# Kernel optimization log

Measured on AMD Instinct MI355X. Metric: run time of the kernel, lower is better.

## Reference

```python
import jax, jax.numpy as jnp
import numpy as np

N, DIM, HID, NCLS, E = 100000, 256, 16, 64, 3200000
NEG_SLOPE = 0.2


def setup_inputs() -> dict:
    key = jax.random.key(0)
    ks = jax.random.split(key, 10)
    x = jax.random.normal(ks[0], (N, DIM), dtype=jnp.float32)
    edge_index = jax.random.randint(ks[1], (2, E), 0, N, dtype=jnp.int64)
    # GATConv params (heads=1): glorot-ish scaled normals
    W1 = jax.random.normal(ks[2], (DIM, HID), dtype=jnp.float32) / np.sqrt(DIM)
    a_src1 = jax.random.normal(ks[3], (HID,), dtype=jnp.float32) / np.sqrt(HID)
    a_dst1 = jax.random.normal(ks[4], (HID,), dtype=jnp.float32) / np.sqrt(HID)
    b1 = jnp.zeros((HID,), dtype=jnp.float32)
    W2 = jax.random.normal(ks[5], (HID, NCLS), dtype=jnp.float32) / np.sqrt(HID)
    a_src2 = jax.random.normal(ks[6], (NCLS,), dtype=jnp.float32) / np.sqrt(NCLS)
    a_dst2 = jax.random.normal(ks[7], (NCLS,), dtype=jnp.float32) / np.sqrt(NCLS)
    b2 = jnp.zeros((NCLS,), dtype=jnp.float32)
    return {"x": x, "edge_index": edge_index, "W1": W1, "a_src1": a_src1,
            "a_dst1": a_dst1, "b1": b1, "W2": W2, "a_src2": a_src2,
            "a_dst2": a_dst2, "b2": b2}


def gat_conv(x, src, dst, W, a_s, a_d, b, n):
    # PyG GATConv, heads=1: h = x W; e_ij = LeakyReLU(a_s.h_j + a_d.h_i)
    h = x @ W                                   # [N, out]
    alpha_s = h @ a_s                           # [N]
    alpha_d = h @ a_d                           # [N]
    e = jax.nn.leaky_relu(alpha_s[src] + alpha_d[dst], NEG_SLOPE)  # [E]
    # softmax over edges grouped by destination node
    m = jax.ops.segment_max(e, dst, num_segments=n)
    m = jnp.where(jnp.isfinite(m), m, 0.0)
    ee = jnp.exp(e - m[dst])
    denom = jax.ops.segment_sum(ee, dst, num_segments=n)
    alpha = ee / denom[dst]                     # self-loops guarantee denom > 0
    out = jax.ops.segment_sum(h[src] * alpha[:, None], dst, num_segments=n)
    return out + b


def reference(x, edge_index, W1, a_src1, a_dst1, b1, W2, a_src2, a_dst2, b2):
    n = x.shape[0]
    loop = jnp.arange(n, dtype=edge_index.dtype)
    src = jnp.concatenate([edge_index[0], loop])  # add self-loops (PyG default)
    dst = jnp.concatenate([edge_index[1], loop])
    h = jax.nn.relu(gat_conv(x, src, dst, W1, a_src1, a_dst1, b1, n))
    # F.dropout treated as identity (inference / deterministic reference)
    out = gat_conv(h, src, dst, W2, a_src2, a_dst2, b2, n)
    return jax.nn.log_softmax(out, axis=1)
```

## Files before the change

kernel.cpp:

```cpp
#include <hip/hip_runtime.h>
#include <hip/hip_fp16.h>


#define DIM 256
#define HID 16
#define NCLS 64
#define NEG 0.2f
#define P1_CHUNK 4096
#define KITER 16
#define CAP 8704

typedef _Float16 f16x8 __attribute__((ext_vector_type(8)));
typedef float f32x4 __attribute__((ext_vector_type(4)));

__device__ __forceinline__ float lrelu(float v) { return v >= 0.f ? v : NEG * v; }

__device__ __forceinline__ uint4 pack_half8(const float* v) {
    __half2 p0 = __floats2half2_rn(v[0], v[1]);
    __half2 p1 = __floats2half2_rn(v[2], v[3]);
    __half2 p2 = __floats2half2_rn(v[4], v[5]);
    __half2 p3 = __floats2half2_rn(v[6], v[7]);
    return make_uint4(*(unsigned*)&p0, *(unsigned*)&p1, *(unsigned*)&p2, *(unsigned*)&p3);
}

__device__ __forceinline__ void unpack_half8(uint4 u, float* f) {
    float2 f0 = __half22float2(*(__half2*)&u.x);
    float2 f1 = __half22float2(*(__half2*)&u.y);
    float2 f2 = __half22float2(*(__half2*)&u.z);
    float2 f3 = __half22float2(*(__half2*)&u.w);
    f[0] = f0.x; f[1] = f0.y; f[2] = f1.x; f[3] = f1.y;
    f[4] = f2.x; f[5] = f2.y; f[6] = f3.x; f[7] = f3.y;
}

__global__ void vsd_kernel(const float* __restrict__ W2, const float* __restrict__ as2,
                           const float* __restrict__ ad2, float* __restrict__ vsd,
                           int* __restrict__ bkt_cnt, int* __restrict__ bkt_cur, int capb) {
    int t = threadIdx.x;
    bkt_cnt[t] = 0;
    bkt_cur[t] = capb ? t * capb : 0;
    if (t < 32) {
        int j = t & 15;
        const float* a = (t < 16) ? as2 : ad2;
        float s = 0.f;
        for (int c = 0; c < NCLS; ++c) s += W2[j * NCLS + c] * a[c];
        vsd[t] = s;
    }
}


__global__ __launch_bounds__(256) void p0_hist(const int* __restrict__ dst, int E,
                                               int* __restrict__ bkt_cnt) {
    __shared__ int hist[512];
    int t = threadIdx.x;
    for (int i = t; i < 512; i += 256) hist[i] = 0;
    __syncthreads();
    int base = blockIdx.x * P1_CHUNK;
#pragma unroll
    for (int k = 0; k < KITER; ++k) {
        int idx = base + k * 256 + t;
        if (idx < E) atomicAdd(&hist[dst[idx] >> 8], 1);
    }
    __syncthreads();
    for (int i = t; i < 512; i += 256)
        if (hist[i]) atomicAdd(&bkt_cnt[i], hist[i]);
}

__global__ void scanb(int* __restrict__ bkt_cnt, int* __restrict__ bkt_cur,
                      int* __restrict__ bkt_base, int nb) {
    __shared__ int lds[512];
    int t = threadIdx.x;
    int v = (t < nb) ? bkt_cnt[t] : 0;
    lds[t] = v;
    __syncthreads();
    for (int o = 1; o < 512; o <<= 1) {
        int x = (t >= o) ? lds[t - o] : 0;
        __syncthreads();
        lds[t] += x;
        __syncthreads();
    }
    if (t < nb) {
        int e = lds[t] - v;
        bkt_base[t] = e;
        bkt_cur[t] = e;
    }
}

struct H1S {
    _Float16 w1t[16][264];
    _Float16 hst[4][16][16];
};

__global__ __launch_bounds__(256) void p1h1_kernel(
    const int* __restrict__ ei, int E, int* __restrict__ bkt_cur,
    int* __restrict__ coarse, int nS, int h1blk, int capb,
    const float* __restrict__ x, const float* __restrict__ W1,
    uint4* __restrict__ h1h, int n) {
    __shared__ union __align__(16) { int hist[512]; H1S h1; } sm;
    int t = threadIdx.x;
    int bid = blockIdx.x;
    int total = nS + h1blk;
    int f0 = (int)(((long long)bid * h1blk) / total);
    int f1 = (int)(((long long)(bid + 1) * h1blk) / total);
    if (f1 == f0) {
        int sb = bid - f0;
        int base = sb * P1_CHUNK;
        int sarr[KITER], darr[KITER];
        for (int i = t; i < 512; i += 256) sm.hist[i] = 0;
        bool e4 = ((E & 3) == 0);
#pragma unroll
        for (int k = 0; k < KITER / 4; ++k) {
            int idx = base + (k * 256 + t) * 4;
            if (e4 && idx + 3 < E) {
                int4 s4 = *(const int4*)&ei[idx];
                int4 d4 = *(const int4*)&ei[E + idx];
                sarr[4 * k] = s4.x; sarr[4 * k + 1] = s4.y;
                sarr[4 * k + 2] = s4.z; sarr[4 * k + 3] = s4.w;
                darr[4 * k] = d4.x; darr[4 * k + 1] = d4.y;
                darr[4 * k + 2] = d4.z; darr[4 * k + 3] = d4.w;
            } else {
#pragma unroll
                for (int j = 0; j < 4; ++j) {
                    int id2 = idx + j;
                    if (id2 < E) { sarr[4 * k + j] = ei[id2]; darr[4 * k + j] = ei[E + id2]; }
                    else darr[4 * k + j] = -1;
                }
            }
        }
        __syncthreads();
#pragma unroll
        for (int k = 0; k < KITER; ++k)
            if (darr[k] >= 0) atomicAdd(&sm.hist[darr[k] >> 8], 1);
        __syncthreads();
        for (int b = t; b < 512; b += 256) {
            int c = sm.hist[b];
            sm.hist[b] = c ? atomicAdd(&bkt_cur[b], c) : 0;
        }
        __syncthreads();
#pragma unroll
        for (int k = 0; k < KITER; ++k) {
            int d = darr[k];
            if (d >= 0) {
                int bk = d >> 8;
                int pos = atomicAdd(&sm.hist[bk], 1);
                if (capb) pos = min(pos, (bk + 1) * capb - 1);
                coarse[pos] = (sarr[k] << 8) | (d & 255);
            }
        }
    } else {
        int hb = f0;
        {
            const float* row = W1 + t * HID;
#pragma unroll
            for (int nn2 = 0; nn2 < 16; ++nn2)
                sm.h1.w1t[nn2][t] = (_Float16)row[nn2];
        }
        __syncthreads();
        int lane = t & 63, wave = t >> 6;
        int q = lane >> 4, nn = lane & 15;
#pragma unroll 1
        for (int it = 0; it < 4; ++it) {
            int nb = hb * 256 + wave * 64 + it * 16;
            int node = nb + nn;
            const float* xr = x + (size_t)min(node, n - 1) * DIM;
            float4 st[16];
#pragma unroll
            for (int s = 0; s < 8; ++s) {
                int kb = s * 32 + q * 8;
                st[2 * s]     = *(const float4*)(xr + kb);
                st[2 * s + 1] = *(const float4*)(xr + kb + 4);
            }
            f32x4 acc = {0.f, 0.f, 0.f, 0.f};
#pragma unroll
            for (int s = 0; s < 8; ++s) {
                int kb = s * 32 + q * 8;
                f16x8 bf = *(const f16x8*)&sm.h1.w1t[nn][kb];
                float4 a0 = st[2 * s], a1 = st[2 * s + 1];
                f16x8 af;
                af[0] = (_Float16)a0.x; af[1] = (_Float16)a0.y;
                af[2] = (_Float16)a0.z; af[3] = (_Float16)a0.w;
                af[4] = (_Float16)a1.x; af[5] = (_Float16)a1.y;
                af[6] = (_Float16)a1.z; af[7] = (_Float16)a1.w;
                acc = __builtin_amdgcn_mfma_f32_16x16x32_f16(af, bf, acc, 0, 0, 0);
            }
            if (nb < n) {
#pragma unroll
                for (int r = 0; r < 4; ++r)
                    sm.h1.hst[wave][q * 4 + r][nn] = (_Float16)acc[r];
                __builtin_amdgcn_s_waitcnt(0);
                if (lane < 32) {
                    int nl = lane >> 1, jq = lane & 1;
                    int nd = nb + nl;
                    if (nd < n)
                        h1h[(size_t)nd * 2 + jq] = *(const uint4*)&sm.h1.hst[wave][nl][jq * 8];
                }
            }
        }
    }
}

__global__ __launch_bounds__(1024) void p2_fine(const int* __restrict__ coarse,
                                                const int* __restrict__ bkt_base,
                                                const int* __restrict__ bkt_cnt,
                                                const int* __restrict__ bkt_cur,
                                                int* __restrict__ csr, int* __restrict__ row_ptr,
                                                int* __restrict__ deg, int n, int capb) {
    __shared__ int cnt[256];
    __shared__ int off[256];
    __shared__ int csr_loc[CAP];
    int b = blockIdx.x;
    int t = threadIdx.x;
    int m, wbase;
    if (capb) {
        int* sc = csr_loc;
        if (t < 512) sc[t] = bkt_cur[t] - t * capb;
        __syncthreads();
        for (int o = 1; o < 512; o <<= 1) {
            int xg = (t >= o && t < 512) ? sc[t - o] : 0;
            __syncthreads();
            if (t < 512) sc[t] += xg;
            __syncthreads();
        }
        m = bkt_cur[b] - b * capb;
        wbase = sc[b] - m;
        __syncthreads();
    } else {
        m = bkt_cnt[b];
        wbase = bkt_base[b];
    }
    int rbase = capb ? b * capb : wbase;
    if (t < 256) cnt[t] = 0;
    __syncthreads();
    for (int i = t; i < m; i += 1024) atomicAdd(&cnt[coarse[rbase + i] & 255], 1);
    __syncthreads();
    int v = 0;
    if (t < 256) { v = cnt[t]; off[t] = v; }
    __syncthreads();
    for (int o = 1; o < 256; o <<= 1) {
        int xg = (t >= o && t < 256) ? off[t - o] : 0;
        __syncthreads();
        if (t < 256) off[t] += xg;
        __syncthreads();
    }
    if (t < 256) {
        int excl = off[t] - v;
        int node = b * 256 + t;
        if (node < n) {
            row_ptr[node] = wbase + excl;
            deg[node] = v;
        }
        cnt[t] = excl;
    }
    __syncthreads();
    if (m <= CAP) {
        for (int i = t; i < m; i += 1024) {
            int rec = coarse[rbase + i];
            int pos = atomicAdd(&cnt[rec & 255], 1);
            csr_loc[pos] = rec >> 8;
        }
        __syncthreads();
        for (int i = t; i < m; i += 1024) csr[wbase + i] = csr_loc[i];
    } else {
        for (int i = t; i < m; i += 1024) {
            int rec = coarse[rbase + i];
            int pos = atomicAdd(&cnt[rec & 255], 1);
            csr[wbase + pos] = rec >> 8;
        }
    }
}


__device__ __forceinline__ void agg_core(
    const uint4* __restrict__ hh, const float* aw, const float* dw,
    int node, int start, int cnt, const int* __restrict__ csr,
    int eq, int jq, float* acc, float* hs, float& denomv) {
    unpack_half8(hh[(size_t)node * 2 + jq], hs);
    float asn = 0.f, adn = 0.f;
#pragma unroll
    for (int i = 0; i < 8; ++i) { asn += hs[i] * aw[i]; adn += hs[i] * dw[i]; }
    asn += __shfl_xor(asn, 1, 64);
    adn += __shfl_xor(adn, 1, 64);
    float adi = adn;
    float w0 = __expf(lrelu(asn + adi));
    float w0s = (eq == 0) ? w0 : 0.f;
#pragma unroll
    for (int i = 0; i < 8; ++i) acc[i] = w0s * hs[i];
    float denom = w0s;
    int s0 = (eq < cnt)      ? csr[start + eq]      : node;
    int s1 = (8 + eq < cnt)  ? csr[start + 8 + eq]  : node;
    int s2 = (16 + eq < cnt) ? csr[start + 16 + eq] : node;
    int s3 = (24 + eq < cnt) ? csr[start + 24 + eq] : node;
    uint4 u0 = hh[(size_t)s0 * 2 + jq];
    uint4 u1 = hh[(size_t)s1 * 2 + jq];
    uint4 u2 = hh[(size_t)s2 * 2 + jq];
    uint4 u3 = hh[(size_t)s3 * 2 + jq];
#pragma unroll 1
    for (int q0 = 0; q0 < cnt; q0 += 32) {
        int nq = q0 + 32;
        int t0 = (nq + eq < cnt)      ? csr[start + nq + eq]      : node;
        int t1 = (nq + 8 + eq < cnt)  ? csr[start + nq + 8 + eq]  : node;
        int t2 = (nq + 16 + eq < cnt) ? csr[start + nq + 16 + eq] : node;
        int t3 = (nq + 24 + eq < cnt) ? csr[start + nq + 24 + eq] : node;
        uint4 v0 = hh[(size_t)t0 * 2 + jq];
        uint4 v1 = hh[(size_t)t1 * 2 + jq];
        uint4 v2 = hh[(size_t)t2 * 2 + jq];
        uint4 v3 = hh[(size_t)t3 * 2 + jq];
        float h[8], p, wv;
        unpack_half8(u0, h);
        p = 0.f;
#pragma unroll
        for (int i = 0; i < 8; ++i) p += h[i] * aw[i];
        p += __shfl_xor(p, 1, 64);
        wv = (q0 + eq < cnt) ? __expf(lrelu(p + adi)) : 0.f;
        denom += wv;
#pragma unroll
        for (int i = 0; i < 8; ++i) acc[i] += wv * h[i];
        unpack_half8(u1, h);
        p = 0.f;
#pragma unroll
        for (int i = 0; i < 8; ++i) p += h[i] * aw[i];
        p += __shfl_xor(p, 1, 64);
        wv = (q0 + 8 + eq < cnt) ? __expf(lrelu(p + adi)) : 0.f;
        denom += wv;
#pragma unroll
        for (int i = 0; i < 8; ++i) acc[i] += wv * h[i];
        unpack_half8(u2, h);
        p = 0.f;
#pragma unroll
        for (int i = 0; i < 8; ++i) p += h[i] * aw[i];
        p += __shfl_xor(p, 1, 64);
        wv = (q0 + 16 + eq < cnt) ? __expf(lrelu(p + adi)) : 0.f;
        denom += wv;
#pragma unroll
        for (int i = 0; i < 8; ++i) acc[i] += wv * h[i];
        unpack_half8(u3, h);
        p = 0.f;
#pragma unroll
        for (int i = 0; i < 8; ++i) p += h[i] * aw[i];
        p += __shfl_xor(p, 1, 64);
        wv = (q0 + 24 + eq < cnt) ? __expf(lrelu(p + adi)) : 0.f;
        denom += wv;
#pragma unroll
        for (int i = 0; i < 8; ++i) acc[i] += wv * h[i];
        u0 = v0; u1 = v1; u2 = v2; u3 = v3;
    }
#pragma unroll
    for (int m = 2; m <= 8; m <<= 1) {
#pragma unroll
        for (int i = 0; i < 8; ++i) acc[i] += __shfl_xor(acc[i], m, 64);
        denom += __shfl_xor(denom, m, 64);
    }
    denomv = denom;
}

__global__ __launch_bounds__(256) void agg1_kernel(
    const uint4* __restrict__ hh,
    const int* __restrict__ row_ptr, const int* __restrict__ deg, const int* __restrict__ csr,
    const float* __restrict__ as1, const float* __restrict__ ad1,
    const float* __restrict__ bias, uint4* __restrict__ outh, int n) {
    int t = threadIdx.x;
    int node = blockIdx.x * 16 + (t >> 4);
    if (node >= n) return;
    int lg = t & 15, jq = lg & 1, eq = lg >> 1;
    float aw[8], dw[8];
#pragma unroll
    for (int i = 0; i < 8; ++i) { aw[i] = as1[jq * 8 + i]; dw[i] = ad1[jq * 8 + i]; }
    float acc[8], hs[8];
    float denom;
    agg_core(hh, aw, dw, node, row_ptr[node], deg[node], csr, eq, jq, acc, hs, denom);
    float inv = 1.f / denom;
    float val[8];
#pragma unroll
    for (int i = 0; i < 8; ++i) val[i] = fmaxf(acc[i] * inv + bias[jq * 8 + i], 0.f);
    if (eq == 0) outh[(size_t)node * 2 + jq] = pack_half8(val);
}

__global__ __launch_bounds__(256) void agg2_final_kernel(
    const uint4* __restrict__ hh,
    const int* __restrict__ row_ptr, const int* __restrict__ deg, const int* __restrict__ csr,
    const float* __restrict__ vsd,
    const float* __restrict__ W2, const float* __restrict__ b2,
    float* __restrict__ out, int n) {
    __shared__ float a2s[16 * HID];
    __shared__ float w2s[HID * NCLS];
    __shared__ float b2s[NCLS];
    int t = threadIdx.x;
    for (int i = t; i < HID * NCLS; i += 256) w2s[i] = W2[i];
    if (t < NCLS) b2s[t] = b2[t];
    int g = t >> 4;
    int node = blockIdx.x * 16 + g;
    int lg = t & 15, jq = lg & 1, eq = lg >> 1;
    if (node < n) {
        float aw[8], dw[8];
#pragma unroll
        for (int i = 0; i < 8; ++i) { aw[i] = vsd[jq * 8 + i]; dw[i] = vsd[16 + jq * 8 + i]; }
        float acc[8], hs[8];
        float denom;
        agg_core(hh, aw, dw, node, row_ptr[node], deg[node], csr, eq, jq, acc, hs, denom);
        float inv = 1.f / denom;
        if (eq == 0) {
            float* dst = &a2s[g * HID + jq * 8];
            *(float4*)dst = make_float4(acc[0] * inv, acc[1] * inv, acc[2] * inv, acc[3] * inv);
            *(float4*)(dst + 4) = make_float4(acc[4] * inv, acc[5] * inv, acc[6] * inv, acc[7] * inv);
        }
    }
    __syncthreads();
    int wv = t >> 6;
    int c = t & 63;
#pragma unroll
    for (int i = 0; i < 4; ++i) {
        int nl = i * 4 + wv;
        int gn = blockIdx.x * 16 + nl;
        if (gn >= n) continue;
        const float* ar = &a2s[nl * HID];
        float v = b2s[c];
#pragma unroll
        for (int j = 0; j < HID; ++j) v += ar[j] * w2s[j * NCLS + c];
        float mx = v;
#pragma unroll
        for (int off = 1; off < 64; off <<= 1) mx = fmaxf(mx, __shfl_xor(mx, off, 64));
        float ex = __expf(v - mx);
        float s = ex;
#pragma unroll
        for (int off = 1; off < 64; off <<= 1) s += __shfl_xor(s, off, 64);
        out[(size_t)gn * NCLS + c] = (v - mx) - __logf(s);
    }
}

extern "C" void kernel_launch(void* const* d_in, const int* in_sizes, int n_in,
                              void* d_out, int out_size, void* d_ws, size_t ws_size,
                              hipStream_t stream) {
    const float* x    = (const float*)d_in[0];
    const int*   ei   = (const int*)d_in[1];
    const float* W1   = (const float*)d_in[2];
    const float* a_s1 = (const float*)d_in[3];
    const float* a_d1 = (const float*)d_in[4];
    const float* b1   = (const float*)d_in[5];
    const float* W2   = (const float*)d_in[6];
    const float* a_s2 = (const float*)d_in[7];
    const float* a_d2 = (const float*)d_in[8];
    const float* b2   = (const float*)d_in[9];
    float* out = (float*)d_out;

    const int N = in_sizes[0] / DIM;
    const int E = in_sizes[1] / 2;
    const int NB = (N + 255) >> 8;
    const int nS = (E + P1_CHUNK - 1) / P1_CHUNK;
    const int h1blk = (N + 255) / 256;

    char* p = (char*)d_ws;
    auto alloc = [&](size_t bytes) {
        char* r = p;
        p += (bytes + 255) & ~(size_t)255;
        return r;
    };
    int*   bkt_cnt  = (int*)alloc(512 * 4);
    int*   bkt_base = (int*)alloc(512 * 4);
    int*   bkt_cur  = (int*)alloc(512 * 4);
    int*   csr      = (int*)alloc((size_t)E * 4);
    int*   row_ptr  = (int*)alloc((size_t)N * 4);
    int*   deg      = (int*)alloc((size_t)N * 4);
    float* vsd      = (float*)alloc(32 * 4);
    uint4* h1h      = (uint4*)alloc((size_t)N * 32);
    uint4* hreluh   = (uint4*)alloc((size_t)N * 32);

    int capb = 10240;
    size_t used = (size_t)(p - (char*)d_ws);
    size_t pad_bytes = (size_t)512 * capb * 4;
    int* coarse;
    if (ws_size - used >= pad_bytes) {
        coarse = (int*)alloc(pad_bytes);
    } else {
        capb = 0;
        coarse = (int*)alloc((size_t)E * 4);
    }

    vsd_kernel<<<1, 512, 0, stream>>>(W2, a_s2, a_d2, vsd, bkt_cnt, bkt_cur, capb);
    if (!capb) {
        p0_hist<<<nS, 256, 0, stream>>>(ei + E, E, bkt_cnt);
        scanb<<<1, 512, 0, stream>>>(bkt_cnt, bkt_cur, bkt_base, NB);
    }
    p1h1_kernel<<<nS + h1blk, 256, 0, stream>>>(ei, E, bkt_cur, coarse, nS, h1blk, capb,
                                                x, W1, h1h, N);
    p2_fine<<<NB, 1024, 0, stream>>>(coarse, bkt_base, bkt_cnt, bkt_cur,
                                     csr, row_ptr, deg, N, capb);
    agg1_kernel<<<(N + 15) / 16, 256, 0, stream>>>(h1h, row_ptr, deg, csr,
                                                   a_s1, a_d1, b1, hreluh, N);
    agg2_final_kernel<<<(N + 15) / 16, 256, 0, stream>>>(hreluh, row_ptr, deg, csr,
                                                         vsd, W2, b2, out, N);
}
```

Before: 289.2 us.

## Fuse fine CSR bucketing with layer-1 aggregation reading neighbor lists from LDS

```diff
diff --git a/kernel.cpp b/kernel.cpp
--- a/kernel.cpp
+++ b/kernel.cpp
@@ -198,80 +198,10 @@
     }
 }
 
-__global__ __launch_bounds__(1024) void p2_fine(const int* __restrict__ coarse,
-                                                const int* __restrict__ bkt_base,
-                                                const int* __restrict__ bkt_cnt,
-                                                const int* __restrict__ bkt_cur,
-                                                int* __restrict__ csr, int* __restrict__ row_ptr,
-                                                int* __restrict__ deg, int n, int capb) {
-    __shared__ int cnt[256];
-    __shared__ int off[256];
-    __shared__ int csr_loc[CAP];
-    int b = blockIdx.x;
-    int t = threadIdx.x;
-    int m, wbase;
-    if (capb) {
-        int* sc = csr_loc;
-        if (t < 512) sc[t] = bkt_cur[t] - t * capb;
-        __syncthreads();
-        for (int o = 1; o < 512; o <<= 1) {
-            int xg = (t >= o && t < 512) ? sc[t - o] : 0;
-            __syncthreads();
-            if (t < 512) sc[t] += xg;
-            __syncthreads();
-        }
-        m = bkt_cur[b] - b * capb;
-        wbase = sc[b] - m;
-        __syncthreads();
-    } else {
-        m = bkt_cnt[b];
-        wbase = bkt_base[b];
-    }
-    int rbase = capb ? b * capb : wbase;
-    if (t < 256) cnt[t] = 0;
-    __syncthreads();
-    for (int i = t; i < m; i += 1024) atomicAdd(&cnt[coarse[rbase + i] & 255], 1);
-    __syncthreads();
-    int v = 0;
-    if (t < 256) { v = cnt[t]; off[t] = v; }
-    __syncthreads();
-    for (int o = 1; o < 256; o <<= 1) {
-        int xg = (t >= o && t < 256) ? off[t - o] : 0;
-        __syncthreads();
-        if (t < 256) off[t] += xg;
-        __syncthreads();
-    }
-    if (t < 256) {
-        int excl = off[t] - v;
-        int node = b * 256 + t;
-        if (node < n) {
-            row_ptr[node] = wbase + excl;
-            deg[node] = v;
-        }
-        cnt[t] = excl;
-    }
-    __syncthreads();
-    if (m <= CAP) {
-        for (int i = t; i < m; i += 1024) {
-            int rec = coarse[rbase + i];
-            int pos = atomicAdd(&cnt[rec & 255], 1);
-            csr_loc[pos] = rec >> 8;
-        }
-        __syncthreads();
-        for (int i = t; i < m; i += 1024) csr[wbase + i] = csr_loc[i];
-    } else {
-        for (int i = t; i < m; i += 1024) {
-            int rec = coarse[rbase + i];
-            int pos = atomicAdd(&cnt[rec & 255], 1);
-            csr[wbase + pos] = rec >> 8;
-        }
-    }
-}
-
 
 __device__ __forceinline__ void agg_core(
     const uint4* __restrict__ hh, const float* aw, const float* dw,
-    int node, int start, int cnt, const int* __restrict__ csr,
+    int node, int start, int cnt, const int* csr,
     int eq, int jq, float* acc, float* hs, float& denomv) {
     unpack_half8(hh[(size_t)node * 2 + jq], hs);
     float asn = 0.f, adn = 0.f;
@@ -352,26 +282,101 @@
     denomv = denom;
 }
 
-__global__ __launch_bounds__(256) void agg1_kernel(
-    const uint4* __restrict__ hh,
-    const int* __restrict__ row_ptr, const int* __restrict__ deg, const int* __restrict__ csr,
-    const float* __restrict__ as1, const float* __restrict__ ad1,
-    const float* __restrict__ bias, uint4* __restrict__ outh, int n) {
-    int t = threadIdx.x;
-    int node = blockIdx.x * 16 + (t >> 4);
-    if (node >= n) return;
+__global__ __launch_bounds__(1024) void p2agg1_kernel(
+    const int* __restrict__ coarse, const int* __restrict__ bkt_base,
+    const int* __restrict__ bkt_cnt, const int* __restrict__ bkt_cur,
+    int* __restrict__ csr, int* __restrict__ row_ptr, int* __restrict__ deg,
+    int n, int capb,
+    const uint4* __restrict__ hh, const float* __restrict__ as1,
+    const float* __restrict__ ad1, const float* __restrict__ bias,
+    uint4* __restrict__ outh) {
+    __shared__ int cnt[256];
+    __shared__ int off[256];
+    __shared__ int lstart[256];
+    __shared__ int ldeg[256];
+    __shared__ int csr_loc[CAP];
+    int b = blockIdx.x;
+    int t = threadIdx.x;
+    int m, wbase;
+    if (capb) {
+        int* sc = csr_loc;
+        if (t < 512) sc[t] = bkt_cur[t] - t * capb;
+        __syncthreads();
+        for (int o = 1; o < 512; o <<= 1) {
+            int xg = (t >= o && t < 512) ? sc[t - o] : 0;
+            __syncthreads();
+            if (t < 512) sc[t] += xg;
+            __syncthreads();
+        }
+        m = bkt_cur[b] - b * capb;
+        wbase = sc[b] - m;
+        __syncthreads();
+    } else {
+        m = bkt_cnt[b];
+        wbase = bkt_base[b];
+    }
+    int rbase = capb ? b * capb : wbase;
+    if (t < 256) cnt[t] = 0;
+    __syncthreads();
+    for (int i = t; i < m; i += 1024) atomicAdd(&cnt[coarse[rbase + i] & 255], 1);
+    __syncthreads();
+    int v = 0;
+    if (t < 256) { v = cnt[t]; off[t] = v; }
+    __syncthreads();
+    for (int o = 1; o < 256; o <<= 1) {
+        int xg = (t >= o && t < 256) ? off[t - o] : 0;
+        __syncthreads();
+        if (t < 256) off[t] += xg;
+        __syncthreads();
+    }
+    bool inlds = (m <= CAP);
+    if (t < 256) {
+        int excl = off[t] - v;
+        int node = b * 256 + t;
+        if (node < n) {
+            row_ptr[node] = wbase + excl;
+            deg[node] = v;
+        }
+        lstart[t] = excl;
+        ldeg[t] = v;
+        cnt[t] = excl;
+    }
+    __syncthreads();
+    if (inlds) {
+        for (int i = t; i < m; i += 1024) {
+            int rec = coarse[rbase + i];
+            int pos = atomicAdd(&cnt[rec & 255], 1);
+            csr_loc[pos] = rec >> 8;
+        }
+        __syncthreads();
+        for (int i = t; i < m; i += 1024) csr[wbase + i] = csr_loc[i];
+    } else {
+        for (int i = t; i < m; i += 1024) {
+            int rec = coarse[rbase + i];
+            int pos = atomicAdd(&cnt[rec & 255], 1);
+            csr[wbase + pos] = rec >> 8;
+        }
+        __syncthreads();
+    }
     int lg = t & 15, jq = lg & 1, eq = lg >> 1;
+    const int* csrp = inlds ? (const int*)csr_loc : (const int*)(csr + wbase);
     float aw[8], dw[8];
 #pragma unroll
     for (int i = 0; i < 8; ++i) { aw[i] = as1[jq * 8 + i]; dw[i] = ad1[jq * 8 + i]; }
-    float acc[8], hs[8];
-    float denom;
-    agg_core(hh, aw, dw, node, row_ptr[node], deg[node], csr, eq, jq, acc, hs, denom);
-    float inv = 1.f / denom;
-    float val[8];
-#pragma unroll
-    for (int i = 0; i < 8; ++i) val[i] = fmaxf(acc[i] * inv + bias[jq * 8 + i], 0.f);
-    if (eq == 0) outh[(size_t)node * 2 + jq] = pack_half8(val);
+#pragma unroll 1
+    for (int pass = 0; pass < 4; ++pass) {
+        int nl = pass * 64 + (t >> 4);
+        int node = b * 256 + nl;
+        if (node >= n) continue;
+        float acc[8], hs[8];
+        float denom;
+        agg_core(hh, aw, dw, node, lstart[nl], ldeg[nl], csrp, eq, jq, acc, hs, denom);
+        float inv = 1.f / denom;
+        float val[8];
+#pragma unroll
+        for (int i = 0; i < 8; ++i) val[i] = fmaxf(acc[i] * inv + bias[jq * 8 + i], 0.f);
+        if (eq == 0) outh[(size_t)node * 2 + jq] = pack_half8(val);
+    }
 }
 
 __global__ __launch_bounds__(256) void agg2_final_kernel(
@@ -481,10 +486,9 @@
     }
     p1h1_kernel<<<nS + h1blk, 256, 0, stream>>>(ei, E, bkt_cur, coarse, nS, h1blk, capb,
                                                 x, W1, h1h, N);
-    p2_fine<<<NB, 1024, 0, stream>>>(coarse, bkt_base, bkt_cnt, bkt_cur,
-                                     csr, row_ptr, deg, N, capb);
-    agg1_kernel<<<(N + 15) / 16, 256, 0, stream>>>(h1h, row_ptr, deg, csr,
-                                                   a_s1, a_d1, b1, hreluh, N);
+    p2agg1_kernel<<<NB, 1024, 0, stream>>>(coarse, bkt_base, bkt_cnt, bkt_cur,
+                                           csr, row_ptr, deg, N, capb,
+                                           h1h, a_s1, a_d1, b1, hreluh);
     agg2_final_kernel<<<(N + 15) / 16, 256, 0, stream>>>(hreluh, row_ptr, deg, csr,
                                                          vsd, W2, b2, out, N);
 }
```

Measured after the change: 300.2 us. +3.8%, slower.

## Replace two-level bucket sort CSR build with per-node atomic histogram and scatter

Applied to the files above, without the earlier changes.

```diff
diff --git a/kernel.cpp b/kernel.cpp
--- a/kernel.cpp
+++ b/kernel.cpp
@@ -6,9 +6,8 @@
 #define HID 16
 #define NCLS 64
 #define NEG 0.2f
-#define P1_CHUNK 4096
-#define KITER 16
-#define CAP 8704
+#define P1_CHUNK 2048
+#define KITER 8
 
 typedef _Float16 f16x8 __attribute__((ext_vector_type(8)));
 typedef float f32x4 __attribute__((ext_vector_type(4)));
@@ -32,13 +31,14 @@
     f[4] = f2.x; f[5] = f2.y; f[6] = f3.x; f[7] = f3.y;
 }
 
-__global__ void vsd_kernel(const float* __restrict__ W2, const float* __restrict__ as2,
-                           const float* __restrict__ ad2, float* __restrict__ vsd,
-                           int* __restrict__ bkt_cnt, int* __restrict__ bkt_cur, int capb) {
-    int t = threadIdx.x;
-    bkt_cnt[t] = 0;
-    bkt_cur[t] = capb ? t * capb : 0;
-    if (t < 32) {
+__global__ __launch_bounds__(1024) void vsd_zero_kernel(
+    const float* __restrict__ W2, const float* __restrict__ as2,
+    const float* __restrict__ ad2, float* __restrict__ vsd,
+    int* __restrict__ deg, int n) {
+    int i = blockIdx.x * 1024 + threadIdx.x;
+    if (i < n) deg[i] = 0;
+    if (blockIdx.x == 0 && threadIdx.x < 32) {
+        int t = threadIdx.x;
         int j = t & 15;
         const float* a = (t < 16) ? as2 : ad2;
         float s = 0.f;
@@ -47,41 +47,60 @@
     }
 }
 
-
-__global__ __launch_bounds__(256) void p0_hist(const int* __restrict__ dst, int E,
-                                               int* __restrict__ bkt_cnt) {
-    __shared__ int hist[512];
+__global__ __launch_bounds__(1024) void hist_kernel(const int* __restrict__ dst, int E,
+                                                    int* __restrict__ deg) {
+    int i4 = (blockIdx.x * 1024 + threadIdx.x) * 4;
+    if (i4 + 3 < E) {
+        int4 d4 = *(const int4*)&dst[i4];
+        atomicAdd(&deg[d4.x], 1);
+        atomicAdd(&deg[d4.y], 1);
+        atomicAdd(&deg[d4.z], 1);
+        atomicAdd(&deg[d4.w], 1);
+    } else {
+        for (int j = 0; j < 4; ++j)
+            if (i4 + j < E) atomicAdd(&deg[dst[i4 + j]], 1);
+    }
+}
+
+__global__ __launch_bounds__(1024) void scan1_kernel(const int* __restrict__ deg,
+                                                     int* __restrict__ row_ptr,
+                                                     int* __restrict__ btot, int n) {
+    __shared__ int arr[1024];
     int t = threadIdx.x;
-    for (int i = t; i < 512; i += 256) hist[i] = 0;
+    int i = blockIdx.x * 1024 + t;
+    int v = (i < n) ? deg[i] : 0;
+    arr[t] = v;
     __syncthreads();
-    int base = blockIdx.x * P1_CHUNK;
-#pragma unroll
-    for (int k = 0; k < KITER; ++k) {
-        int idx = base + k * 256 + t;
-        if (idx < E) atomicAdd(&hist[dst[idx] >> 8], 1);
-    }
+    for (int o = 1; o < 1024; o <<= 1) {
+        int x = (t >= o) ? arr[t - o] : 0;
+        __syncthreads();
+        arr[t] += x;
+        __syncthreads();
+    }
+    if (i < n) row_ptr[i] = arr[t] - v;
+    if (t == 1023) btot[blockIdx.x] = arr[1023];
+}
+
+__global__ __launch_bounds__(1024) void finalize_kernel(const int* __restrict__ btot,
+                                                        int* __restrict__ row_ptr,
+                                                        int* __restrict__ cursor,
+                                                        int n, int nblk) {
+    __shared__ int bs[128];
+    int t = threadIdx.x;
+    if (t < 128) bs[t] = (t < nblk) ? btot[t] : 0;
     __syncthreads();
-    for (int i = t; i < 512; i += 256)
-        if (hist[i]) atomicAdd(&bkt_cnt[i], hist[i]);
-}
-
-__global__ void scanb(int* __restrict__ bkt_cnt, int* __restrict__ bkt_cur,
-                      int* __restrict__ bkt_base, int nb) {
-    __shared__ int lds[512];
-    int t = threadIdx.x;
-    int v = (t < nb) ? bkt_cnt[t] : 0;
-    lds[t] = v;
-    __syncthreads();
-    for (int o = 1; o < 512; o <<= 1) {
-        int x = (t >= o) ? lds[t - o] : 0;
+    for (int o = 1; o < 128; o <<= 1) {
+        int x = (t >= o && t < 128) ? bs[t - o] : 0;
         __syncthreads();
-        lds[t] += x;
+        if (t < 128) bs[t] += x;
         __syncthreads();
     }
-    if (t < nb) {
-        int e = lds[t] - v;
-        bkt_base[t] = e;
-        bkt_cur[t] = e;
+    int base = (blockIdx.x == 0) ? 0 : bs[blockIdx.x - 1];
+    int i = blockIdx.x * 1024 + t;
+    if (i < n) {
+        int rp = row_ptr[i] + base;
+        row_ptr[i] = rp;
+        cursor[i] = rp;
     }
 }
 
@@ -90,12 +109,12 @@
     _Float16 hst[4][16][16];
 };
 
-__global__ __launch_bounds__(256) void p1h1_kernel(
-    const int* __restrict__ ei, int E, int* __restrict__ bkt_cur,
-    int* __restrict__ coarse, int nS, int h1blk, int capb,
+__global__ __launch_bounds__(256) void scat_h1_kernel(
+    const int* __restrict__ ei, int E, int* __restrict__ cursor,
+    int* __restrict__ csr, int nS, int h1blk,
     const float* __restrict__ x, const float* __restrict__ W1,
     uint4* __restrict__ h1h, int n) {
-    __shared__ union __align__(16) { int hist[512]; H1S h1; } sm;
+    __shared__ H1S sm;
     int t = threadIdx.x;
     int bid = blockIdx.x;
     int total = nS + h1blk;
@@ -104,8 +123,6 @@
     if (f1 == f0) {
         int sb = bid - f0;
         int base = sb * P1_CHUNK;
-        int sarr[KITER], darr[KITER];
-        for (int i = t; i < 512; i += 256) sm.hist[i] = 0;
         bool e4 = ((E & 3) == 0);
 #pragma unroll
         for (int k = 0; k < KITER / 4; ++k) {
@@ -113,37 +130,23 @@
             if (e4 && idx + 3 < E) {
                 int4 s4 = *(const int4*)&ei[idx];
                 int4 d4 = *(const int4*)&ei[E + idx];
-                sarr[4 * k] = s4.x; sarr[4 * k + 1] = s4.y;
-                sarr[4 * k + 2] = s4.z; sarr[4 * k + 3] = s4.w;
-                darr[4 * k] = d4.x; darr[4 * k + 1] = d4.y;
-                darr[4 * k + 2] = d4.z; darr[4 * k + 3] = d4.w;
+                int p0 = atomicAdd(&cursor[d4.x], 1);
+                int p1 = atomicAdd(&cursor[d4.y], 1);
+                int p2 = atomicAdd(&cursor[d4.z], 1);
+                int p3 = atomicAdd(&cursor[d4.w], 1);
+                csr[p0] = s4.x;
+                csr[p1] = s4.y;
+                csr[p2] = s4.z;
+                csr[p3] = s4.w;
             } else {
 #pragma unroll
                 for (int j = 0; j < 4; ++j) {
                     int id2 = idx + j;
-                    if (id2 < E) { sarr[4 * k + j] = ei[id2]; darr[4 * k + j] = ei[E + id2]; }
-                    else darr[4 * k + j] = -1;
+                    if (id2 < E) {
+                        int s = ei[id2], d = ei[E + id2];
+                        csr[atomicAdd(&cursor[d], 1)] = s;
+                    }
                 }
-            }
-        }
-        __syncthreads();
-#pragma unroll
-        for (int k = 0; k < KITER; ++k)
-            if (darr[k] >= 0) atomicAdd(&sm.hist[darr[k] >> 8], 1);
-        __syncthreads();
-        for (int b = t; b < 512; b += 256) {
-            int c = sm.hist[b];
-            sm.hist[b] = c ? atomicAdd(&bkt_cur[b], c) : 0;
-        }
-        __syncthreads();
-#pragma unroll
-        for (int k = 0; k < KITER; ++k) {
-            int d = darr[k];
-            if (d >= 0) {
-                int bk = d >> 8;
-                int pos = atomicAdd(&sm.hist[bk], 1);
-                if (capb) pos = min(pos, (bk + 1) * capb - 1);
-                coarse[pos] = (sarr[k] << 8) | (d & 255);
             }
         }
     } else {
@@ -152,7 +155,7 @@
             const float* row = W1 + t * HID;
 #pragma unroll
             for (int nn2 = 0; nn2 < 16; ++nn2)
-                sm.h1.w1t[nn2][t] = (_Float16)row[nn2];
+                sm.w1t[nn2][t] = (_Float16)row[nn2];
         }
         __syncthreads();
         int lane = t & 63, wave = t >> 6;
@@ -173,7 +176,7 @@
 #pragma unroll
             for (int s = 0; s < 8; ++s) {
                 int kb = s * 32 + q * 8;
-                f16x8 bf = *(const f16x8*)&sm.h1.w1t[nn][kb];
+                f16x8 bf = *(const f16x8*)&sm.w1t[nn][kb];
                 float4 a0 = st[2 * s], a1 = st[2 * s + 1];
                 f16x8 af;
                 af[0] = (_Float16)a0.x; af[1] = (_Float16)a0.y;
@@ -185,85 +188,15 @@
             if (nb < n) {
 #pragma unroll
                 for (int r = 0; r < 4; ++r)
-                    sm.h1.hst[wave][q * 4 + r][nn] = (_Float16)acc[r];
+                    sm.hst[wave][q * 4 + r][nn] = (_Float16)acc[r];
                 __builtin_amdgcn_s_waitcnt(0);
                 if (lane < 32) {
                     int nl = lane >> 1, jq = lane & 1;
                     int nd = nb + nl;
                     if (nd < n)
-                        h1h[(size_t)nd * 2 + jq] = *(const uint4*)&sm.h1.hst[wave][nl][jq * 8];
+                        h1h[(size_t)nd * 2 + jq] = *(const uint4*)&sm.hst[wave][nl][jq * 8];
                 }
             }
-        }
-    }
-}
-
-__global__ __launch_bounds__(1024) void p2_fine(const int* __restrict__ coarse,
-                                                const int* __restrict__ bkt_base,
-                                                const int* __restrict__ bkt_cnt,
-                                                const int* __restrict__ bkt_cur,
-                                                int* __restrict__ csr, int* __restrict__ row_ptr,
-                                                int* __restrict__ deg, int n, int capb) {
-    __shared__ int cnt[256];
-    __shared__ int off[256];
-    __shared__ int csr_loc[CAP];
-    int b = blockIdx.x;
-    int t = threadIdx.x;
-    int m, wbase;
-    if (capb) {
-        int* sc = csr_loc;
-        if (t < 512) sc[t] = bkt_cur[t] - t * capb;
-        __syncthreads();
-        for (int o = 1; o < 512; o <<= 1) {
-            int xg = (t >= o && t < 512) ? sc[t - o] : 0;
-            __syncthreads();
-            if (t < 512) sc[t] += xg;
-            __syncthreads();
-        }
-        m = bkt_cur[b] - b * capb;
-        wbase = sc[b] - m;
-        __syncthreads();
-    } else {
-        m = bkt_cnt[b];
-        wbase = bkt_base[b];
-    }
-    int rbase = capb ? b * capb : wbase;
-    if (t < 256) cnt[t] = 0;
-    __syncthreads();
-    for (int i = t; i < m; i += 1024) atomicAdd(&cnt[coarse[rbase + i] & 255], 1);
-    __syncthreads();
-    int v = 0;
-    if (t < 256) { v = cnt[t]; off[t] = v; }
-    __syncthreads();
-    for (int o = 1; o < 256; o <<= 1) {
-        int xg = (t >= o && t < 256) ? off[t - o] : 0;
-        __syncthreads();
-        if (t < 256) off[t] += xg;
-        __syncthreads();
-    }
-    if (t < 256) {
-        int excl = off[t] - v;
-        int node = b * 256 + t;
-        if (node < n) {
-            row_ptr[node] = wbase + excl;
-            deg[node] = v;
-        }
-        cnt[t] = excl;
-    }
-    __syncthreads();
-    if (m <= CAP) {
-        for (int i = t; i < m; i += 1024) {
-            int rec = coarse[rbase + i];
-            int pos = atomicAdd(&cnt[rec & 255], 1);
-            csr_loc[pos] = rec >> 8;
-        }
-        __syncthreads();
-        for (int i = t; i < m; i += 1024) csr[wbase + i] = csr_loc[i];
-    } else {
-        for (int i = t; i < m; i += 1024) {
-            int rec = coarse[rbase + i];
-            int pos = atomicAdd(&cnt[rec & 255], 1);
-            csr[wbase + pos] = rec >> 8;
         }
     }
 }
@@ -443,9 +376,10 @@
 
     const int N = in_sizes[0] / DIM;
     const int E = in_sizes[1] / 2;
-    const int NB = (N + 255) >> 8;
     const int nS = (E + P1_CHUNK - 1) / P1_CHUNK;
     const int h1blk = (N + 255) / 256;
+    const int nscan = (N + 1023) / 1024;
+    const int nhist = (E / 4 + 1023) / 1024 + 1;
 
     char* p = (char*)d_ws;
     auto alloc = [&](size_t bytes) {
@@ -453,36 +387,21 @@
         p += (bytes + 255) & ~(size_t)255;
         return r;
     };
-    int*   bkt_cnt  = (int*)alloc(512 * 4);
-    int*   bkt_base = (int*)alloc(512 * 4);
-    int*   bkt_cur  = (int*)alloc(512 * 4);
+    int*   deg      = (int*)alloc((size_t)N * 4);
+    int*   row_ptr  = (int*)alloc((size_t)N * 4);
+    int*   cursor   = (int*)alloc((size_t)N * 4);
+    int*   btot     = (int*)alloc(256 * 4);
+    float* vsd      = (float*)alloc(32 * 4);
     int*   csr      = (int*)alloc((size_t)E * 4);
-    int*   row_ptr  = (int*)alloc((size_t)N * 4);
-    int*   deg      = (int*)alloc((size_t)N * 4);
-    float* vsd      = (float*)alloc(32 * 4);
     uint4* h1h      = (uint4*)alloc((size_t)N * 32);
     uint4* hreluh   = (uint4*)alloc((size_t)N * 32);
 
-    int capb = 10240;
-    size_t used = (size_t)(p - (char*)d_ws);
-    size_t pad_bytes = (size_t)512 * capb * 4;
-    int* coarse;
-    if (ws_size - used >= pad_bytes) {
-        coarse = (int*)alloc(pad_bytes);
-    } else {
-        capb = 0;
-        coarse = (int*)alloc((size_t)E * 4);
-    }
-
-    vsd_kernel<<<1, 512, 0, stream>>>(W2, a_s2, a_d2, vsd, bkt_cnt, bkt_cur, capb);
-    if (!capb) {
-        p0_hist<<<nS, 256, 0, stream>>>(ei + E, E, bkt_cnt);
-        scanb<<<1, 512, 0, stream>>>(bkt_cnt, bkt_cur, bkt_base, NB);
-    }
-    p1h1_kernel<<<nS + h1blk, 256, 0, stream>>>(ei, E, bkt_cur, coarse, nS, h1blk, capb,
-                                                x, W1, h1h, N);
-    p2_fine<<<NB, 1024, 0, stream>>>(coarse, bkt_base, bkt_cnt, bkt_cur,
-                                     csr, row_ptr, deg, N, capb);
+    vsd_zero_kernel<<<nscan, 1024, 0, stream>>>(W2, a_s2, a_d2, vsd, deg, N);
+    hist_kernel<<<nhist, 1024, 0, stream>>>(ei + E, E, deg);
+    scan1_kernel<<<nscan, 1024, 0, stream>>>(deg, row_ptr, btot, N);
+    finalize_kernel<<<nscan, 1024, 0, stream>>>(btot, row_ptr, cursor, N, nscan);
+    scat_h1_kernel<<<nS + h1blk, 256, 0, stream>>>(ei, E, cursor, csr, nS, h1blk,
+                                                   x, W1, h1h, N);
     agg1_kernel<<<(N + 15) / 16, 256, 0, stream>>>(h1h, row_ptr, deg, csr,
                                                    a_s1, a_d1, b1, hreluh, N);
     agg2_final_kernel<<<(N + 15) / 16, 256, 0, stream>>>(hreluh, row_ptr, deg, csr,
```

Measured after the change: 539.9 us. +86.7%, slower.
